# Kernel optimization log

Hardware: AMD Instinct MI355X
Metric: run time of the kernel (lower is better)

The kernel has to match this reference:

```python
import jax, jax.numpy as jnp
import numpy as np

DIM = 768
NUM_HEADS = 12
HEAD_DIM = DIM // NUM_HEADS
SCALE = HEAD_DIM ** -0.5


def setup_inputs() -> dict:
    key = jax.random.key(0)
    k1, k2, k3, k4 = jax.random.split(key, 4)
    B, N, C = 4, 2048, DIM
    x = jax.random.normal(k1, (B, N, C), dtype=jnp.float32)
    # nn.Linear(dim, 3*dim, bias=False): weight shape (3C, C), y = x @ W^T
    w_qkv = jax.random.normal(k2, (3 * C, C), dtype=jnp.float32) * (C ** -0.5)
    # nn.Linear(dim, dim) with default bias=True
    w_proj = jax.random.normal(k3, (C, C), dtype=jnp.float32) * (C ** -0.5)
    b_proj = jax.random.normal(k4, (C,), dtype=jnp.float32) * 0.02
    return {"x": x, "w_qkv": w_qkv, "w_proj": w_proj, "b_proj": b_proj}


def reference(x, w_qkv, w_proj, b_proj):
    B, N, C = x.shape
    H, D = NUM_HEADS, HEAD_DIM
    qkv = jnp.einsum('bnc,oc->bno', x, w_qkv)  # (B, N, 3C)
    qkv = qkv.reshape(B, N, 3, H, D).transpose(2, 0, 3, 1, 4)  # (3, B, H, N, D)
    q, k, v = qkv[0], qkv[1], qkv[2]
    attn = jnp.einsum('bhnd,bhmd->bhnm', q, k) * jnp.float32(SCALE)  # (B,H,N,N)
    attn = jax.nn.softmax(attn, axis=-1)
    out = jnp.einsum('bhnm,bhmd->bhnd', attn, v)  # (B,H,N,D)
    out = out.transpose(0, 2, 1, 3).reshape(B, N, C)
    out = jnp.einsum('bnc,oc->bno', out, w_proj) + b_proj
    return out
```

## Files before the change

### kernel.cpp

```cpp
#include <hip/hip_runtime.h>
#include <math.h>

#define B_ 4
#define N_ 2048
#define C_ 768
#define H_ 12
#define D_ 64
#define QKSCALE_ 0.18033688011112042f

typedef unsigned short u16;
typedef unsigned int u32;
typedef short s16x8 __attribute__((ext_vector_type(8)));
typedef float f32x4 __attribute__((ext_vector_type(4)));
typedef u32 u32x2 __attribute__((ext_vector_type(2)));

__device__ __forceinline__ u16 f2bf(float f) {
    union { float f; u32 u; } v; v.f = f;
    u32 r = (v.u + 0x7fffu + ((v.u >> 16) & 1u)) >> 16;
    return (u16)r;
}

__device__ __forceinline__ u32 pkbf(float a, float b) {
    union { float f; u32 u; } ua, ub; ua.f = a; ub.f = b;
    u32 ra = ua.u + 0x7fffu + ((ua.u >> 16) & 1u);
    u32 rb = ub.u + 0x7fffu + ((ub.u >> 16) & 1u);
    return __builtin_amdgcn_perm(rb, ra, 0x07060302u);
}

__device__ __forceinline__ void gl_lds16(const u16* g, u16* l) {
    __builtin_amdgcn_global_load_lds(
        (__attribute__((address_space(1))) void*)g,
        (__attribute__((address_space(3))) void*)l, 16, 0, 0);
}

__global__ __launch_bounds__(256) void cvt_bf16(const float4* __restrict__ src,
                                                ushort4* __restrict__ dst, int n4)
{
    int i = blockIdx.x * blockDim.x + threadIdx.x;
    const int stride = gridDim.x * blockDim.x;
    for (; i < n4; i += stride) {
        float4 v = src[i];
        ushort4 o;
        o.x = f2bf(v.x); o.y = f2bf(v.y); o.z = f2bf(v.z); o.w = f2bf(v.w);
        dst[i] = o;
    }
}

template<int BM, bool OUT_BF16, bool BIAS, bool QSCALE>
__global__ __launch_bounds__(256) void gemm_mfma(const u16* __restrict__ A,
                                                 const u16* __restrict__ Bm,
                                                 const float* __restrict__ bias,
                                                 void* __restrict__ Cout,
                                                 int M, int N, int K)
{
    constexpr int MF = BM / 32;
    __shared__ __align__(16) u16 As[BM * 32];
    __shared__ __align__(16) u16 Bs[128 * 32];
    const int tid  = threadIdx.x;
    const int wv   = tid >> 6;
    const int lane = tid & 63;
    const int lr   = lane & 15;
    const int lq   = lane >> 4;
    const int wm   = (wv >> 1) * (BM / 2);
    const int wn   = (wv & 1) * 64;
    const int row0 = blockIdx.y * BM, col0 = blockIdx.x * 128;

    f32x4 acc[MF][4];
    #pragma unroll
    for (int i = 0; i < MF; i++)
        #pragma unroll
        for (int j = 0; j < 4; j++) { f32x4 z = {0.f,0.f,0.f,0.f}; acc[i][j] = z; }

    const int srow   = lane >> 2;
    const int schunk = (((lane & 3) ^ ((lane >> 3) & 3)) * 8);

    const int arow_base = (BM == 128) ? 32 * wv : 16 * wv;
    const u16* gA0 = A + (size_t)(row0 + arow_base + srow) * K + schunk;
    const u16* gA1 = gA0 + (size_t)16 * K;
    const u16* gB0 = Bm + (size_t)(col0 + 32 * wv + srow) * K + schunk;
    const u16* gB1 = gB0 + (size_t)16 * K;
    u16* lA0 = As + arow_base * 32;
    u16* lA1 = lA0 + 16 * 32;
    u16* lB0 = Bs + (32 * wv) * 32;
    u16* lB1 = lB0 + 16 * 32;

    const int ppos = (lq ^ ((lr >> 1) & 3)) * 8;

    for (int k0 = 0; k0 < K; k0 += 32) {
        gl_lds16(gA0 + k0, lA0);
        if (BM == 128) gl_lds16(gA1 + k0, lA1);
        gl_lds16(gB0 + k0, lB0);
        gl_lds16(gB1 + k0, lB1);
        __syncthreads();
        s16x8 af[MF], bfr[4];
        #pragma unroll
        for (int i = 0; i < MF; i++)
            af[i] = *(const s16x8*)&As[(wm + 16*i + lr) * 32 + ppos];
        #pragma unroll
        for (int j = 0; j < 4; j++)
            bfr[j] = *(const s16x8*)&Bs[(wn + 16*j + lr) * 32 + ppos];
        #pragma unroll
        for (int i = 0; i < MF; i++)
            #pragma unroll
            for (int j = 0; j < 4; j++)
                acc[i][j] = __builtin_amdgcn_mfma_f32_16x16x32_bf16(af[i], bfr[j], acc[i][j], 0, 0, 0);
        __syncthreads();
    }

    #pragma unroll
    for (int i = 0; i < MF; i++) {
        #pragma unroll
        for (int j = 0; j < 4; j++) {
            const int col = col0 + wn + 16*j + lr;
            float bv = BIAS ? bias[col] : 0.f;
            #pragma unroll
            for (int r = 0; r < 4; r++) {
                const int row = row0 + wm + 16*i + lq*4 + r;
                float v = acc[i][j][r] + bv;
                if (QSCALE && col < C_) v *= QKSCALE_;
                if (OUT_BF16) ((u16*)Cout)[(size_t)row * N + col] = f2bf(v);
                else          ((float*)Cout)[(size_t)row * N + col] = v;
            }
        }
    }
}

__global__ __launch_bounds__(256, 3) void attn_mfma(const u16* __restrict__ qkv,
                                                    u16* __restrict__ attout)
{
    __shared__ __align__(16) u16 Ks[64][72];
    __shared__ __align__(16) u16 Vt[64][72];
    __shared__ __align__(16) u16 Ps[128][72];

    const int tid  = threadIdx.x;
    const int wv   = tid >> 6;
    const int lane = tid & 63;
    const int lr   = lane & 15;
    const int lq   = lane >> 4;
    const int n0   = blockIdx.x * 128;
    const int bh   = blockIdx.y, b = bh / H_, h = bh % H_;
    const size_t rs = 3 * C_;

    const u16* Qg = qkv + ((size_t)b * N_ + n0) * rs + h * D_;
    const u16* Kg = qkv + ((size_t)b * N_) * rs + C_ + h * D_;
    const u16* Vg = Kg + C_;

    s16x8 qf[2][2];
    #pragma unroll
    for (int iq = 0; iq < 2; iq++)
        #pragma unroll
        for (int kk = 0; kk < 2; kk++)
            qf[iq][kk] = *(const s16x8*)(Qg + (size_t)(32*wv + 16*iq + lr) * rs + kk*32 + lq*8);

    f32x4 oacc[2][4];
    float li[2] = {0.f, 0.f};
    #pragma unroll
    for (int i = 0; i < 2; i++)
        #pragma unroll
        for (int j = 0; j < 4; j++) { f32x4 z = {0.f,0.f,0.f,0.f}; oacc[i][j] = z; }

    const int skey = tid >> 2, sd0 = (tid & 3) * 16;
    const int vc = tid & 7, vp = tid >> 3;
    const int vkey0 = 2 * vp, vd0 = vc * 8;
    const int vcol0 = (vkey0 + 8 * vc) & 63;

    s16x8 kr0, kr1, vr0, vr1;
    {
        const u16* kp = Kg + (size_t)skey * rs + sd0;
        kr0 = *(const s16x8*)kp; kr1 = *(const s16x8*)(kp + 8);
        const u16* vp2 = Vg + (size_t)vkey0 * rs + vd0;
        vr0 = *(const s16x8*)vp2; vr1 = *(const s16x8*)(vp2 + rs);
    }

    for (int t = 0; t < N_ / 64; t++) {
        __syncthreads();
        *(s16x8*)&Ks[skey][sd0]     = kr0;
        *(s16x8*)&Ks[skey][sd0 + 8] = kr1;
        #pragma unroll
        for (int u = 0; u < 8; u++) {
            u32 pk = (u32)(u16)vr0[u] | ((u32)(u16)vr1[u] << 16);
            *(u32*)&Vt[vd0 + u][vcol0] = pk;
        }
        __syncthreads();
        if (t + 1 < N_ / 64) {
            const u16* kp = Kg + (size_t)((t+1)*64 + skey) * rs + sd0;
            kr0 = *(const s16x8*)kp; kr1 = *(const s16x8*)(kp + 8);
            const u16* vp2 = Vg + (size_t)((t+1)*64 + vkey0) * rs + vd0;
            vr0 = *(const s16x8*)vp2; vr1 = *(const s16x8*)(vp2 + rs);
        }

        f32x4 st[4][2];
        #pragma unroll
        for (int jk = 0; jk < 4; jk++)
            #pragma unroll
            for (int iq = 0; iq < 2; iq++) { f32x4 z = {0.f,0.f,0.f,0.f}; st[jk][iq] = z; }
        #pragma unroll
        for (int kk = 0; kk < 2; kk++) {
            s16x8 kf[4];
            #pragma unroll
            for (int jk = 0; jk < 4; jk++)
                kf[jk] = *(const s16x8*)&Ks[16*jk + lr][kk*32 + lq*8];
            #pragma unroll
            for (int jk = 0; jk < 4; jk++) {
                st[jk][0] = __builtin_amdgcn_mfma_f32_16x16x32_bf16(kf[jk], qf[0][kk], st[jk][0], 0, 0, 0);
                st[jk][1] = __builtin_amdgcn_mfma_f32_16x16x32_bf16(kf[jk], qf[1][kk], st[jk][1], 0, 0, 0);
            }
        }

        #pragma unroll
        for (int jk = 0; jk < 4; jk++)
            #pragma unroll
            for (int iq = 0; iq < 2; iq++) {
                const float p0 = __builtin_amdgcn_exp2f(st[jk][iq][0]);
                const float p1 = __builtin_amdgcn_exp2f(st[jk][iq][1]);
                const float p2 = __builtin_amdgcn_exp2f(st[jk][iq][2]);
                const float p3 = __builtin_amdgcn_exp2f(st[jk][iq][3]);
                li[iq] += (p0 + p1) + (p2 + p3);
                u32x2 w;
                w.x = pkbf(p0, p1);
                w.y = pkbf(p2, p3);
                *(u32x2*)&Ps[32*wv + 16*iq + lr][16*jk + 4*lq] = w;
            }

        #pragma unroll
        for (int kk = 0; kk < 2; kk++) {
            s16x8 ap0 = *(const s16x8*)&Ps[32*wv      + lr][kk*32 + lq*8];
            s16x8 ap1 = *(const s16x8*)&Ps[32*wv + 16 + lr][kk*32 + lq*8];
            #pragma unroll
            for (int j2 = 0; j2 < 4; j2++) {
                const int pb = ((kk*4 + lq) + 2*j2 + (lr >> 3)) & 7;
                s16x8 bv = *(const s16x8*)&Vt[16*j2 + lr][pb * 8];
                oacc[0][j2] = __builtin_amdgcn_mfma_f32_16x16x32_bf16(ap0, bv, oacc[0][j2], 0, 0, 0);
                oacc[1][j2] = __builtin_amdgcn_mfma_f32_16x16x32_bf16(ap1, bv, oacc[1][j2], 0, 0, 0);
            }
        }
    }

    #pragma unroll
    for (int iq = 0; iq < 2; iq++) {
        li[iq] += __shfl_xor(li[iq], 16);
        li[iq] += __shfl_xor(li[iq], 32);
    }
    #pragma unroll
    for (int iq = 0; iq < 2; iq++) {
        #pragma unroll
        for (int r = 0; r < 4; r++) {
            const float inv = 1.f / __shfl(li[iq], 4*lq + r);
            const int row = n0 + 32*wv + 16*iq + 4*lq + r;
            #pragma unroll
            for (int j2 = 0; j2 < 4; j2++)
                attout[((size_t)(b * N_ + row)) * C_ + h * D_ + 16*j2 + lr] =
                    f2bf(oacc[iq][j2][r] * inv);
        }
    }
}

extern "C" void kernel_launch(void* const* d_in, const int* in_sizes, int n_in,
                              void* d_out, int out_size, void* d_ws, size_t ws_size,
                              hipStream_t stream) {
    const float* x      = (const float*)d_in[0];
    const float* w_qkv  = (const float*)d_in[1];
    const float* w_proj = (const float*)d_in[2];
    const float* b_proj = (const float*)d_in[3];
    float* out = (float*)d_out;

    const int NX   = B_ * N_ * C_;
    const int NWQ  = 3 * C_ * C_;
    const int NWP  = C_ * C_;
    const int NQKV = B_ * N_ * 3 * C_;

    u16* xb   = (u16*)d_ws;
    u16* wqb  = xb + NX;
    u16* wpb  = wqb + NWQ;
    u16* qkvb = wpb + NWP;
    u16* attb = qkvb + NQKV;

    dim3 blk(256);

    cvt_bf16<<<512, blk, 0, stream>>>((const float4*)x, (ushort4*)xb, NX / 4);
    cvt_bf16<<<256, blk, 0, stream>>>((const float4*)w_qkv, (ushort4*)wqb, NWQ / 4);
    cvt_bf16<<<128, blk, 0, stream>>>((const float4*)w_proj, (ushort4*)wpb, NWP / 4);

    const int M = B_ * N_;
    gemm_mfma<128, true, false, true><<<dim3((3*C_)/128, M/128), blk, 0, stream>>>(
        xb, wqb, nullptr, qkvb, M, 3*C_, C_);

    attn_mfma<<<dim3(N_/128, B_ * H_), blk, 0, stream>>>(qkvb, attb);

    gemm_mfma<64, false, true, false><<<dim3(C_/128, M/64), blk, 0, stream>>>(
        attb, wpb, b_proj, out, M, C_, C_);
}
```

Baseline: 232.9 us.

## Double-buffer GEMM LDS tiles, fuse bf16 conversions, use hardware bf16 pack

The GEMM kernel now keeps two LDS buffers and issues the global-to-LDS loads for the next K-slice before computing on the current one. This drops one barrier per iteration and is meant to hide load latency. The three separate fp32-to-bf16 conversion launches become a single kernel, which saves launch overhead. pkbf uses the hardware packed bf16 conversion builtin when the compiler provides it. Doubling LDS use may lower occupancy, and the single barrier relies on the async LDS loads completing before that barrier.

```diff
diff --git a/kernel.cpp b/kernel.cpp
--- a/kernel.cpp
+++ b/kernel.cpp
@@ -20,12 +20,20 @@
     return (u16)r;
 }
 
+#if __has_builtin(__builtin_amdgcn_cvt_pk_bf16_f32)
+__device__ __forceinline__ u32 pkbf(float a, float b) {
+    auto r = __builtin_amdgcn_cvt_pk_bf16_f32(a, b);
+    u32 u; __builtin_memcpy(&u, &r, 4);
+    return u;
+}
+#else
 __device__ __forceinline__ u32 pkbf(float a, float b) {
     union { float f; u32 u; } ua, ub; ua.f = a; ub.f = b;
     u32 ra = ua.u + 0x7fffu + ((ua.u >> 16) & 1u);
     u32 rb = ub.u + 0x7fffu + ((ub.u >> 16) & 1u);
     return __builtin_amdgcn_perm(rb, ra, 0x07060302u);
 }
+#endif
 
 __device__ __forceinline__ void gl_lds16(const u16* g, u16* l) {
     __builtin_amdgcn_global_load_lds(
@@ -33,16 +41,28 @@
         (__attribute__((address_space(3))) void*)l, 16, 0, 0);
 }
 
-__global__ __launch_bounds__(256) void cvt_bf16(const float4* __restrict__ src,
-                                                ushort4* __restrict__ dst, int n4)
+#define NX4_  (B_ * N_ * C_ / 4)
+#define NWQ4_ (3 * C_ * C_ / 4)
+#define NWP4_ (C_ * C_ / 4)
+__global__ __launch_bounds__(256) void cvt_all(const float4* __restrict__ x,
+                                               const float4* __restrict__ wq,
+                                               const float4* __restrict__ wp,
+                                               ushort4* __restrict__ xb,
+                                               ushort4* __restrict__ wqb,
+                                               ushort4* __restrict__ wpb)
 {
+    const int tot = NX4_ + NWQ4_ + NWP4_;
     int i = blockIdx.x * blockDim.x + threadIdx.x;
     const int stride = gridDim.x * blockDim.x;
-    for (; i < n4; i += stride) {
-        float4 v = src[i];
+    for (; i < tot; i += stride) {
+        const float4* s; ushort4* d; int j;
+        if (i < NX4_)              { s = x;  d = xb;  j = i; }
+        else if (i < NX4_ + NWQ4_) { s = wq; d = wqb; j = i - NX4_; }
+        else                       { s = wp; d = wpb; j = i - NX4_ - NWQ4_; }
+        float4 v = s[j];
         ushort4 o;
         o.x = f2bf(v.x); o.y = f2bf(v.y); o.z = f2bf(v.z); o.w = f2bf(v.w);
-        dst[i] = o;
+        d[j] = o;
     }
 }
 
@@ -54,8 +74,9 @@
                                                  int M, int N, int K)
 {
     constexpr int MF = BM / 32;
-    __shared__ __align__(16) u16 As[BM * 32];
-    __shared__ __align__(16) u16 Bs[128 * 32];
+    constexpr int ASZ = BM * 32, BSZ = 128 * 32;
+    __shared__ __align__(16) u16 As[2 * ASZ];
+    __shared__ __align__(16) u16 Bs[2 * BSZ];
     const int tid  = threadIdx.x;
     const int wv   = tid >> 6;
     const int lane = tid & 63;
@@ -79,32 +100,42 @@
     const u16* gA1 = gA0 + (size_t)16 * K;
     const u16* gB0 = Bm + (size_t)(col0 + 32 * wv + srow) * K + schunk;
     const u16* gB1 = gB0 + (size_t)16 * K;
-    u16* lA0 = As + arow_base * 32;
-    u16* lA1 = lA0 + 16 * 32;
-    u16* lB0 = Bs + (32 * wv) * 32;
-    u16* lB1 = lB0 + 16 * 32;
+    const int aoff0 = arow_base * 32, aoff1 = aoff0 + 16 * 32;
+    const int boff0 = (32 * wv) * 32, boff1 = boff0 + 16 * 32;
 
     const int ppos = (lq ^ ((lr >> 1) & 3)) * 8;
-
-    for (int k0 = 0; k0 < K; k0 += 32) {
-        gl_lds16(gA0 + k0, lA0);
-        if (BM == 128) gl_lds16(gA1 + k0, lA1);
-        gl_lds16(gB0 + k0, lB0);
-        gl_lds16(gB1 + k0, lB1);
+    const int nIter = K / 32;
+
+    gl_lds16(gA0, As + aoff0);
+    if (BM == 128) gl_lds16(gA1, As + aoff1);
+    gl_lds16(gB0, Bs + boff0);
+    gl_lds16(gB1, Bs + boff1);
+
+    for (int t = 0; t < nIter; t++) {
+        const int cur = t & 1;
         __syncthreads();
+        if (t + 1 < nIter) {
+            const int k1 = (t + 1) * 32;
+            const int nb = cur ^ 1;
+            gl_lds16(gA0 + k1, As + nb * ASZ + aoff0);
+            if (BM == 128) gl_lds16(gA1 + k1, As + nb * ASZ + aoff1);
+            gl_lds16(gB0 + k1, Bs + nb * BSZ + boff0);
+            gl_lds16(gB1 + k1, Bs + nb * BSZ + boff1);
+        }
+        const u16* __restrict__ Ac = As + cur * ASZ;
+        const u16* __restrict__ Bc = Bs + cur * BSZ;
         s16x8 af[MF], bfr[4];
         #pragma unroll
         for (int i = 0; i < MF; i++)
-            af[i] = *(const s16x8*)&As[(wm + 16*i + lr) * 32 + ppos];
+            af[i] = *(const s16x8*)&Ac[(wm + 16*i + lr) * 32 + ppos];
         #pragma unroll
         for (int j = 0; j < 4; j++)
-            bfr[j] = *(const s16x8*)&Bs[(wn + 16*j + lr) * 32 + ppos];
+            bfr[j] = *(const s16x8*)&Bc[(wn + 16*j + lr) * 32 + ppos];
         #pragma unroll
         for (int i = 0; i < MF; i++)
             #pragma unroll
             for (int j = 0; j < 4; j++)
                 acc[i][j] = __builtin_amdgcn_mfma_f32_16x16x32_bf16(af[i], bfr[j], acc[i][j], 0, 0, 0);
-        __syncthreads();
     }
 
     #pragma unroll
@@ -277,9 +308,9 @@
 
     dim3 blk(256);
 
-    cvt_bf16<<<512, blk, 0, stream>>>((const float4*)x, (ushort4*)xb, NX / 4);
-    cvt_bf16<<<256, blk, 0, stream>>>((const float4*)w_qkv, (ushort4*)wqb, NWQ / 4);
-    cvt_bf16<<<128, blk, 0, stream>>>((const float4*)w_proj, (ushort4*)wpb, NWP / 4);
+    cvt_all<<<768, blk, 0, stream>>>((const float4*)x, (const float4*)w_qkv,
+                                     (const float4*)w_proj,
+                                     (ushort4*)xb, (ushort4*)wqb, (ushort4*)wpb);
 
     const int M = B_ * N_;
     gemm_mfma<128, true, false, true><<<dim3((3*C_)/128, M/128), blk, 0, stream>>>(
```

New measurement: 227.5 us. 1.02x faster.
